# Kernel optimization log

Hardware: AMD Instinct MI355X
Metric: run time of the kernel (lower is better)

Reference implementation:

```python
import jax, jax.numpy as jnp
import numpy as np

N_ENT, N_REL, E_DIM, R_DIM, K, B = 100000, 64, 128, 128, 32, 16384


def _lookup_maxnorm(table, ids):
    # torch nn.Embedding(max_norm=1): rows with L2 norm > 1 are renormed to 1 at lookup
    x = table[ids]
    n = jnp.linalg.norm(x, axis=-1, keepdims=True)
    return x * jnp.minimum(1.0, 1.0 / jnp.maximum(n, 1e-12))


def setup_inputs() -> dict:
    key = jax.random.key(0)
    ks = jax.random.split(key, 10)
    xavier = lambda k, shp: jax.random.uniform(k, shp, jnp.float32, -1.0, 1.0) * np.sqrt(6.0 / (shp[0] + shp[1]))
    return {
        "idx": jax.random.randint(ks[0], (B,), 0, N_ENT),
        "adj_ent": jax.random.randint(ks[1], (N_ENT, K), 0, N_ENT),
        "adj_rel": jax.random.randint(ks[2], (N_ENT, K), 0, N_REL),
        "ent_table": xavier(ks[3], (N_ENT, E_DIM)),
        "rel_table": xavier(ks[4], (N_REL, R_DIM)),
        "Wr_w": xavier(ks[5], (R_DIM, E_DIM)),
        "Wr_b": jnp.zeros((R_DIM,), jnp.float32),
        "W1_w": xavier(ks[6], (E_DIM, E_DIM)),
        "W1_b": jnp.zeros((E_DIM,), jnp.float32),
        "W2_w": xavier(ks[7], (E_DIM, E_DIM)),
        "W2_b": jnp.zeros((E_DIM,), jnp.float32),
    }


def reference(idx, adj_ent, adj_rel, ent_table, rel_table, Wr_w, Wr_b, W1_w, W1_b, W2_w, W2_b):
    idx = jnp.clip(idx, 0, N_ENT - 1)
    e_ids = adj_ent[idx]                      # [B, K]
    r_ids = adj_rel[idx]                      # [B, K]
    t = _lookup_maxnorm(ent_table, e_ids)     # [B, K, E]
    r = _lookup_maxnorm(rel_table, r_ids)     # [B, K, R]
    h = _lookup_maxnorm(ent_table, idx)       # [B, E]
    # GAT message pass
    hr = h @ Wr_w.T + Wr_b                    # [B, R]
    tr = t @ Wr_w.T + Wr_b                    # [B, K, R]
    score = jnp.sum(jnp.tanh(hr[:, None, :] + r) * tr, axis=-1, keepdims=True)  # [B, K, 1]
    att = jax.nn.softmax(score, axis=1)
    Nh = jnp.sum(t * att, axis=1)             # [B, E]
    # Bi-Interaction aggregate
    leaky = lambda x: jax.nn.leaky_relu(x, 0.2)
    return leaky((h + Nh) @ W1_w.T + W1_b) + leaky((h * Nh) @ W2_w.T + W2_b)
```

## Files before the change

### kernel.cpp

```cpp
#include <hip/hip_runtime.h>
#include <hip/hip_fp16.h>
#include <math.h>

#define N_ENT 100000
#define N_REL 64
#define DIM   128
#define KNB   32
#define BATCH 16384
#define STRIPS (N_ENT / 16)

typedef _Float16 f16;
typedef __attribute__((ext_vector_type(2))) _Float16 f16x2;
typedef __attribute__((ext_vector_type(8))) _Float16 f16x8;
typedef __attribute__((ext_vector_type(4))) float floatx4;

__device__ __forceinline__ int clamp_id(int id) {
    return id < 0 ? 0 : (id > N_ENT - 1 ? N_ENT - 1 : id);
}

__device__ __forceinline__ float poly_tanh(float x) {
    const float x2 = x * x;
    return x * fmaf(x2, fmaf(x2, 0.13333334f, -0.33333334f), 1.0f);
}

__device__ __forceinline__ f16x2 h2v(__half2 h) {
    union { __half2 h; f16x2 v; } u; u.h = h; return u.v;
}

__global__ __launch_bounds__(256) void k_small(
    const float* __restrict__ Wr, const float* __restrict__ W1,
    const float* __restrict__ W2, f16* __restrict__ Wr16,
    f16* __restrict__ W116, f16* __restrict__ W216,
    const float* __restrict__ rel, __half2* __restrict__ REL2)
{
    if (blockIdx.x < 64) {
        const int t = blockIdx.x * 256 + threadIdx.x;
        Wr16[t] = (f16)Wr[t];
        W116[t] = (f16)W1[t];
        W216[t] = (f16)W2[t];
    } else {
        const int lane = threadIdx.x & 63;
        const int row  = (blockIdx.x - 64) * 4 + (threadIdx.x >> 6);
        const float2 x = *(const float2*)(rel + row * DIM + 2 * lane);
        float ss = x.x * x.x + x.y * x.y;
        #pragma unroll
        for (int m = 1; m < 64; m <<= 1) ss += __shfl_xor(ss, m);
        const float s = fminf(1.0f, 1.0f / fmaxf(sqrtf(ss), 1e-12f));
        REL2[row * 64 + lane] = __floats2half2_rn(x.x * s, x.y * s);
    }
}

__global__ __launch_bounds__(256, 4) void k_pre(
    const float* __restrict__ ent, const f16* __restrict__ B,
    const float* __restrict__ bias, f16* __restrict__ TR16,
    f16* __restrict__ N16)
{
    __shared__ f16 Bs[32 * 512];
    const int wid  = threadIdx.x >> 6;
    const int lane = threadIdx.x & 63;
    const int m = lane & 15, quad = lane >> 4;

    #pragma unroll
    for (int i = 0; i < 8; ++i) {
        const int s  = wid * 8 + i;
        const int ct = s >> 2, kt = s & 3;
        const f16* gsrc = B + (size_t)(ct * 16 + m) * DIM + kt * 32 + quad * 8;
        __builtin_amdgcn_global_load_lds(
            (const __attribute__((address_space(1))) unsigned int*)gsrc,
            (__attribute__((address_space(3))) unsigned int*)(Bs + s * 512),
            16, 0, 0);
    }

    const int wstrip = (blockIdx.x * 4 + wid) * 2;
    const int s0 = wstrip     < STRIPS ? wstrip     : STRIPS - 1;
    const int s1 = wstrip + 1 < STRIPS ? wstrip + 1 : STRIPS - 1;

    const float* __restrict__ src0 = ent + (size_t)(s0 * 16 + m) * DIM + quad * 8;
    const float* __restrict__ src1 = ent + (size_t)(s1 * 16 + m) * DIM + quad * 8;
    float x0[4][8], x1[4][8];
    #pragma unroll
    for (int kt = 0; kt < 4; ++kt) {
        *(float4*)&x0[kt][0] = *(const float4*)(src0 + kt * 32);
        *(float4*)&x0[kt][4] = *(const float4*)(src0 + kt * 32 + 4);
    }
    #pragma unroll
    for (int kt = 0; kt < 4; ++kt) {
        *(float4*)&x1[kt][0] = *(const float4*)(src1 + kt * 32);
        *(float4*)&x1[kt][4] = *(const float4*)(src1 + kt * 32 + 4);
    }
    __builtin_amdgcn_sched_barrier(0);

    float ss0 = 0.0f;
    #pragma unroll
    for (int kt = 0; kt < 4; ++kt)
        #pragma unroll
        for (int j = 0; j < 8; ++j) ss0 = fmaf(x0[kt][j], x0[kt][j], ss0);
    ss0 += __shfl_xor(ss0, 16);
    ss0 += __shfl_xor(ss0, 32);
    const float sc0 = fminf(1.0f, 1.0f / fmaxf(sqrtf(ss0), 1e-12f));
    f16x8 a0[4];
    {
        f16* __restrict__ ndst = N16 + (size_t)(s0 * 16 + m) * DIM + quad * 8;
        #pragma unroll
        for (int kt = 0; kt < 4; ++kt) {
            f16x8 av;
            #pragma unroll
            for (int j = 0; j < 8; ++j) av[j] = (f16)(x0[kt][j] * sc0);
            a0[kt] = av;
            *(f16x8*)(ndst + kt * 32) = av;
        }
    }

    float ss1 = 0.0f;
    #pragma unroll
    for (int kt = 0; kt < 4; ++kt)
        #pragma unroll
        for (int j = 0; j < 8; ++j) ss1 = fmaf(x1[kt][j], x1[kt][j], ss1);
    ss1 += __shfl_xor(ss1, 16);
    ss1 += __shfl_xor(ss1, 32);
    const float sc1 = fminf(1.0f, 1.0f / fmaxf(sqrtf(ss1), 1e-12f));
    f16x8 a1[4];
    {
        f16* __restrict__ ndst = N16 + (size_t)(s1 * 16 + m) * DIM + quad * 8;
        #pragma unroll
        for (int kt = 0; kt < 4; ++kt) {
            f16x8 av;
            #pragma unroll
            for (int j = 0; j < 8; ++j) av[j] = (f16)(x1[kt][j] * sc1);
            a1[kt] = av;
            *(f16x8*)(ndst + kt * 32) = av;
        }
    }

    __syncthreads();

    #pragma unroll
    for (int ct = 0; ct < 8; ++ct) {
        floatx4 acc0 = {0.0f, 0.0f, 0.0f, 0.0f};
        floatx4 acc1 = {0.0f, 0.0f, 0.0f, 0.0f};
        #pragma unroll
        for (int kt = 0; kt < 4; ++kt) {
            const f16x8 b = *(const f16x8*)(Bs + (ct * 4 + kt) * 512 + lane * 8);
            acc0 = __builtin_amdgcn_mfma_f32_16x16x32_f16(a0[kt], b, acc0, 0, 0, 0);
            acc1 = __builtin_amdgcn_mfma_f32_16x16x32_f16(a1[kt], b, acc1, 0, 0, 0);
        }
        const float bb = bias[ct * 16 + m];
        #pragma unroll
        for (int r = 0; r < 4; ++r) {
            TR16[(size_t)(s0 * 16 + quad * 4 + r) * DIM + ct * 16 + m] = (f16)(acc0[r] + bb);
            TR16[(size_t)(s1 * 16 + quad * 4 + r) * DIM + ct * 16 + m] = (f16)(acc1[r] + bb);
        }
    }
}

__global__ __launch_bounds__(256, 4) void k_sa(
    const int* __restrict__ idx, const int* __restrict__ adj_ent,
    const int* __restrict__ adj_rel, const __half2* __restrict__ TR2,
    const __half2* __restrict__ N2, const __half2* __restrict__ REL2,
    __half2* __restrict__ U2, __half2* __restrict__ V2)
{
    const int wid  = threadIdx.x >> 6;
    const int lane = threadIdx.x & 63;
    const int b = blockIdx.x * 4 + wid;

    const int id = clamp_id(idx[b]);
    const __half2 hr2 = TR2[(size_t)id * 64 + lane];
    const float2 h  = __half22float2(N2[(size_t)id * 64 + lane]);
    const int eL = adj_ent[(size_t)id * KNB + (lane & 31)];
    const int rL = adj_rel[(size_t)id * KNB + (lane & 31)];

    unsigned int tnd[KNB];
    #pragma unroll
    for (int k = 0; k < KNB; ++k) {
        const int e = __builtin_amdgcn_readlane(eL, k);
        tnd[k] = *((const unsigned int*)N2 + (size_t)e * 64 + lane);
    }

    const __half2 C1 = __float2half2_rn(-0.33333334f);
    const __half2 C2 = __float2half2_rn(0.13333334f);
    float p[KNB];
    #pragma unroll
    for (int k = 0; k < KNB; ++k) {
        const int e = __builtin_amdgcn_readlane(eL, k);
        const int r = __builtin_amdgcn_readlane(rL, k);
        const __half2 tr2 = TR2[(size_t)e * 64 + lane];
        const __half2 rn2 = REL2[r * 64 + lane];
        const __half2 x  = __hadd2(hr2, rn2);
        const __half2 xx = __hmul2(x, x);
        __half2 q = __hfma2(xx, C2, C1);
        q = __hmul2(q, xx);
        const __half2 mm = __hfma2(x, q, x);
#if __has_builtin(__builtin_amdgcn_fdot2)
        p[k] = __builtin_amdgcn_fdot2(h2v(mm), h2v(tr2), 0.0f, false);
#else
        const float2 mf = __half22float2(mm);
        const float2 tf = __half22float2(tr2);
        p[k] = mf.x * tf.x + mf.y * tf.y;
#endif
    }

    #pragma unroll
    for (int step = 0; step < 5; ++step) {
        const int half = 16 >> step;
        const int mask = 1 << step;
        const bool hi_lane = (lane & mask) != 0;
        #pragma unroll
        for (int i = 0; i < 16; ++i) {
            if (i >= half) break;
            const float lo = p[i], hi = p[i + half];
            const float send = hi_lane ? lo : hi;
            const float recv = __shfl_xor(send, mask);
            p[i] = (hi_lane ? hi : lo) + recv;
        }
    }
    const float sc = p[0] + __shfl_xor(p[0], 32);

    const float ex = __expf(sc);
    float tt = ex;
    #pragma unroll
    for (int m = 1; m < 32; m <<= 1) tt += __shfl_xor(tt, m);
    const float attL = ex * __builtin_amdgcn_rcpf(tt);

    float nh0 = 0.0f, nh1 = 0.0f;
    #pragma unroll
    for (int k = 0; k < KNB; ++k) {
        const float a = __uint_as_float(
            __builtin_amdgcn_readlane(__float_as_uint(attL), k));
        const float2 t = __half22float2(*(const __half2*)&tnd[k]);
        nh0 = fmaf(a, t.x, nh0);
        nh1 = fmaf(a, t.y, nh1);
    }

    U2[(size_t)b * 64 + lane] = __floats2half2_rn(h.x + nh0, h.y + nh1);
    V2[(size_t)b * 64 + lane] = __floats2half2_rn(h.x * nh0, h.y * nh1);
}

__global__ __launch_bounds__(256, 4) void k_gemm_out(
    const f16* __restrict__ U, const f16* __restrict__ V,
    const f16* __restrict__ W1h, const float* __restrict__ b1,
    const f16* __restrict__ W2h, const float* __restrict__ b2,
    float* __restrict__ out)
{
    const int wid  = threadIdx.x >> 6;
    const int lane = threadIdx.x & 63;
    const int g = blockIdx.x * 4 + wid;
    const int strip = g >> 1;
    const int ct0 = (g & 1) * 4;
    const int row0 = strip * 16;
    const int m = lane & 15, quad = lane >> 4;

    f16x8 au[4], av[4];
    #pragma unroll
    for (int kt = 0; kt < 4; ++kt) {
        au[kt] = *(const f16x8*)(U + (size_t)(row0 + m) * DIM + kt * 32 + quad * 8);
        av[kt] = *(const f16x8*)(V + (size_t)(row0 + m) * DIM + kt * 32 + quad * 8);
    }

    #pragma unroll
    for (int c = 0; c < 4; ++c) {
        const int ct = ct0 + c;
        floatx4 accU = {0.0f, 0.0f, 0.0f, 0.0f};
        floatx4 accV = {0.0f, 0.0f, 0.0f, 0.0f};
        #pragma unroll
        for (int kt = 0; kt < 4; ++kt) {
            const f16x8 bu = *(const f16x8*)(W1h + (size_t)(ct * 16 + m) * DIM + kt * 32 + quad * 8);
            const f16x8 bv = *(const f16x8*)(W2h + (size_t)(ct * 16 + m) * DIM + kt * 32 + quad * 8);
            accU = __builtin_amdgcn_mfma_f32_16x16x32_f16(au[kt], bu, accU, 0, 0, 0);
            accV = __builtin_amdgcn_mfma_f32_16x16x32_f16(av[kt], bv, accV, 0, 0, 0);
        }
        const float bb1 = b1[ct * 16 + m];
        const float bb2 = b2[ct * 16 + m];
        #pragma unroll
        for (int r = 0; r < 4; ++r) {
            const float x = accU[r] + bb1;
            const float y = accV[r] + bb2;
            const float lx = x > 0.0f ? x : 0.2f * x;
            const float ly = y > 0.0f ? y : 0.2f * y;
            out[(size_t)(row0 + quad * 4 + r) * DIM + ct * 16 + m] = lx + ly;
        }
    }
}

extern "C" void kernel_launch(void* const* d_in, const int* in_sizes, int n_in,
                              void* d_out, int out_size, void* d_ws, size_t ws_size,
                              hipStream_t stream) {
    (void)in_sizes; (void)n_in; (void)out_size; (void)ws_size;
    const int*   idx     = (const int*)d_in[0];
    const int*   adj_ent = (const int*)d_in[1];
    const int*   adj_rel = (const int*)d_in[2];
    const float* ent     = (const float*)d_in[3];
    const float* rel     = (const float*)d_in[4];
    const float* Wr_w    = (const float*)d_in[5];
    const float* Wr_b    = (const float*)d_in[6];
    const float* W1_w    = (const float*)d_in[7];
    const float* W1_b    = (const float*)d_in[8];
    const float* W2_w    = (const float*)d_in[9];
    const float* W2_b    = (const float*)d_in[10];
    float* out = (float*)d_out;

    char* ws = (char*)d_ws;
    f16* N16   = (f16*)(ws);
    f16* TR16  = (f16*)(ws + 25600000);
    f16* REL16 = (f16*)(ws + 51200000);
    f16* U16   = (f16*)(ws + 51216384);
    f16* V16   = (f16*)(ws + 55410688);
    f16* Wr16  = (f16*)(ws + 59604992);
    f16* W116  = (f16*)(ws + 59637760);
    f16* W216  = (f16*)(ws + 59670528);

    k_small<<<dim3(80), dim3(256), 0, stream>>>(Wr_w, W1_w, W2_w, Wr16, W116, W216,
                                                rel, (__half2*)REL16);
    k_pre<<<dim3((STRIPS + 7) / 8), dim3(256), 0, stream>>>(ent, Wr16, Wr_b,
                                                            TR16, N16);
    k_sa<<<dim3(BATCH / 4), dim3(256), 0, stream>>>(idx, adj_ent, adj_rel,
                                                    (const __half2*)TR16,
                                                    (const __half2*)N16,
                                                    (const __half2*)REL16,
                                                    (__half2*)U16, (__half2*)V16);
    k_gemm_out<<<dim3(512), dim3(256), 0, stream>>>(U16, V16, W116, W1_b,
                                                    W216, W2_b, out);
}
```

Before: 184.5 us.

## Fuse attention aggregation with output GEMM through swizzled shared memory

Merges the per-row attention/aggregation kernel with the bi-interaction output GEMM. Each 256-thread block now processes 16 batch rows: every wave handles 4 rows sequentially, writes U and V into XOR-swizzled LDS tiles, then after a barrier computes 2 column tiles of the MFMA GEMM. This removes the global round trip for U/V and one kernel launch. In exchange the grid shrinks by 4x to 1024 blocks, and the sequential per-wave loop plus the barrier may reduce latency hiding on the gather-heavy phase.

```diff
diff --git a/kernel.cpp b/kernel.cpp
--- a/kernel.cpp
+++ b/kernel.cpp
@@ -16,11 +16,6 @@
 
 __device__ __forceinline__ int clamp_id(int id) {
     return id < 0 ? 0 : (id > N_ENT - 1 ? N_ENT - 1 : id);
-}
-
-__device__ __forceinline__ float poly_tanh(float x) {
-    const float x2 = x * x;
-    return x * fmaf(x2, fmaf(x2, 0.13333334f, -0.33333334f), 1.0f);
 }
 
 __device__ __forceinline__ f16x2 h2v(__half2 h) {
@@ -153,112 +148,113 @@
     }
 }
 
-__global__ __launch_bounds__(256, 4) void k_sa(
+__global__ __launch_bounds__(256, 4) void k_sag(
     const int* __restrict__ idx, const int* __restrict__ adj_ent,
     const int* __restrict__ adj_rel, const __half2* __restrict__ TR2,
     const __half2* __restrict__ N2, const __half2* __restrict__ REL2,
-    __half2* __restrict__ U2, __half2* __restrict__ V2)
-{
-    const int wid  = threadIdx.x >> 6;
-    const int lane = threadIdx.x & 63;
-    const int b = blockIdx.x * 4 + wid;
-
-    const int id = clamp_id(idx[b]);
-    const __half2 hr2 = TR2[(size_t)id * 64 + lane];
-    const float2 h  = __half22float2(N2[(size_t)id * 64 + lane]);
-    const int eL = adj_ent[(size_t)id * KNB + (lane & 31)];
-    const int rL = adj_rel[(size_t)id * KNB + (lane & 31)];
-
-    unsigned int tnd[KNB];
-    #pragma unroll
-    for (int k = 0; k < KNB; ++k) {
-        const int e = __builtin_amdgcn_readlane(eL, k);
-        tnd[k] = *((const unsigned int*)N2 + (size_t)e * 64 + lane);
-    }
-
-    const __half2 C1 = __float2half2_rn(-0.33333334f);
-    const __half2 C2 = __float2half2_rn(0.13333334f);
-    float p[KNB];
-    #pragma unroll
-    for (int k = 0; k < KNB; ++k) {
-        const int e = __builtin_amdgcn_readlane(eL, k);
-        const int r = __builtin_amdgcn_readlane(rL, k);
-        const __half2 tr2 = TR2[(size_t)e * 64 + lane];
-        const __half2 rn2 = REL2[r * 64 + lane];
-        const __half2 x  = __hadd2(hr2, rn2);
-        const __half2 xx = __hmul2(x, x);
-        __half2 q = __hfma2(xx, C2, C1);
-        q = __hmul2(q, xx);
-        const __half2 mm = __hfma2(x, q, x);
-#if __has_builtin(__builtin_amdgcn_fdot2)
-        p[k] = __builtin_amdgcn_fdot2(h2v(mm), h2v(tr2), 0.0f, false);
-#else
-        const float2 mf = __half22float2(mm);
-        const float2 tf = __half22float2(tr2);
-        p[k] = mf.x * tf.x + mf.y * tf.y;
-#endif
-    }
-
-    #pragma unroll
-    for (int step = 0; step < 5; ++step) {
-        const int half = 16 >> step;
-        const int mask = 1 << step;
-        const bool hi_lane = (lane & mask) != 0;
-        #pragma unroll
-        for (int i = 0; i < 16; ++i) {
-            if (i >= half) break;
-            const float lo = p[i], hi = p[i + half];
-            const float send = hi_lane ? lo : hi;
-            const float recv = __shfl_xor(send, mask);
-            p[i] = (hi_lane ? hi : lo) + recv;
-        }
-    }
-    const float sc = p[0] + __shfl_xor(p[0], 32);
-
-    const float ex = __expf(sc);
-    float tt = ex;
-    #pragma unroll
-    for (int m = 1; m < 32; m <<= 1) tt += __shfl_xor(tt, m);
-    const float attL = ex * __builtin_amdgcn_rcpf(tt);
-
-    float nh0 = 0.0f, nh1 = 0.0f;
-    #pragma unroll
-    for (int k = 0; k < KNB; ++k) {
-        const float a = __uint_as_float(
-            __builtin_amdgcn_readlane(__float_as_uint(attL), k));
-        const float2 t = __half22float2(*(const __half2*)&tnd[k]);
-        nh0 = fmaf(a, t.x, nh0);
-        nh1 = fmaf(a, t.y, nh1);
-    }
-
-    U2[(size_t)b * 64 + lane] = __floats2half2_rn(h.x + nh0, h.y + nh1);
-    V2[(size_t)b * 64 + lane] = __floats2half2_rn(h.x * nh0, h.y * nh1);
-}
-
-__global__ __launch_bounds__(256, 4) void k_gemm_out(
-    const f16* __restrict__ U, const f16* __restrict__ V,
     const f16* __restrict__ W1h, const float* __restrict__ b1,
     const f16* __restrict__ W2h, const float* __restrict__ b2,
     float* __restrict__ out)
 {
+    __shared__ f16 Us[16 * DIM];
+    __shared__ f16 Vs[16 * DIM];
     const int wid  = threadIdx.x >> 6;
     const int lane = threadIdx.x & 63;
-    const int g = blockIdx.x * 4 + wid;
-    const int strip = g >> 1;
-    const int ct0 = (g & 1) * 4;
-    const int row0 = strip * 16;
+    const int row0 = blockIdx.x * 16;
+
+    const __half2 C1 = __float2half2_rn(-0.33333334f);
+    const __half2 C2 = __float2half2_rn(0.13333334f);
+
+    #pragma unroll 1
+    for (int e4 = 0; e4 < 4; ++e4) {
+        const int r = wid * 4 + e4;
+        const int b = row0 + r;
+        const int id = clamp_id(idx[b]);
+        const __half2 hr2 = TR2[(size_t)id * 64 + lane];
+        const float2 h  = __half22float2(N2[(size_t)id * 64 + lane]);
+        const int eL = adj_ent[(size_t)id * KNB + (lane & 31)];
+        const int rL = adj_rel[(size_t)id * KNB + (lane & 31)];
+
+        unsigned int tnd[KNB];
+        #pragma unroll
+        for (int k = 0; k < KNB; ++k) {
+            const int e = __builtin_amdgcn_readlane(eL, k);
+            tnd[k] = *((const unsigned int*)N2 + (size_t)e * 64 + lane);
+        }
+
+        float p[KNB];
+        #pragma unroll
+        for (int k = 0; k < KNB; ++k) {
+            const int e = __builtin_amdgcn_readlane(eL, k);
+            const int rr = __builtin_amdgcn_readlane(rL, k);
+            const __half2 tr2 = TR2[(size_t)e * 64 + lane];
+            const __half2 rn2 = REL2[rr * 64 + lane];
+            const __half2 x  = __hadd2(hr2, rn2);
+            const __half2 xx = __hmul2(x, x);
+            __half2 q = __hfma2(xx, C2, C1);
+            q = __hmul2(q, xx);
+            const __half2 mm = __hfma2(x, q, x);
+#if __has_builtin(__builtin_amdgcn_fdot2)
+            p[k] = __builtin_amdgcn_fdot2(h2v(mm), h2v(tr2), 0.0f, false);
+#else
+            const float2 mf = __half22float2(mm);
+            const float2 tf = __half22float2(tr2);
+            p[k] = mf.x * tf.x + mf.y * tf.y;
+#endif
+        }
+
+        #pragma unroll
+        for (int step = 0; step < 5; ++step) {
+            const int half = 16 >> step;
+            const int mask = 1 << step;
+            const bool hi_lane = (lane & mask) != 0;
+            #pragma unroll
+            for (int i = 0; i < 16; ++i) {
+                if (i >= half) break;
+                const float lo = p[i], hi = p[i + half];
+                const float send = hi_lane ? lo : hi;
+                const float recv = __shfl_xor(send, mask);
+                p[i] = (hi_lane ? hi : lo) + recv;
+            }
+        }
+        const float sc = p[0] + __shfl_xor(p[0], 32);
+
+        const float ex = __expf(sc);
+        float tt = ex;
+        #pragma unroll
+        for (int m2 = 1; m2 < 32; m2 <<= 1) tt += __shfl_xor(tt, m2);
+        const float attL = ex * __builtin_amdgcn_rcpf(tt);
+
+        float nh0 = 0.0f, nh1 = 0.0f;
+        #pragma unroll
+        for (int k = 0; k < KNB; ++k) {
+            const float a = __uint_as_float(
+                __builtin_amdgcn_readlane(__float_as_uint(attL), k));
+            const float2 t = __half22float2(*(const __half2*)&tnd[k]);
+            nh0 = fmaf(a, t.x, nh0);
+            nh1 = fmaf(a, t.y, nh1);
+        }
+
+        const int chunk = lane >> 2;
+        const int boff = r * 256 + ((chunk ^ (r & 7)) << 4) + (lane & 3) * 4;
+        *(__half2*)((char*)Us + boff) = __floats2half2_rn(h.x + nh0, h.y + nh1);
+        *(__half2*)((char*)Vs + boff) = __floats2half2_rn(h.x * nh0, h.y * nh1);
+    }
+
+    __syncthreads();
+
     const int m = lane & 15, quad = lane >> 4;
-
     f16x8 au[4], av[4];
     #pragma unroll
     for (int kt = 0; kt < 4; ++kt) {
-        au[kt] = *(const f16x8*)(U + (size_t)(row0 + m) * DIM + kt * 32 + quad * 8);
-        av[kt] = *(const f16x8*)(V + (size_t)(row0 + m) * DIM + kt * 32 + quad * 8);
-    }
-
-    #pragma unroll
-    for (int c = 0; c < 4; ++c) {
-        const int ct = ct0 + c;
+        const int off = m * 256 + (((kt * 4 + quad) ^ (m & 7)) << 4);
+        au[kt] = *(const f16x8*)((const char*)Us + off);
+        av[kt] = *(const f16x8*)((const char*)Vs + off);
+    }
+
+    #pragma unroll
+    for (int c = 0; c < 2; ++c) {
+        const int ct = wid * 2 + c;
         floatx4 accU = {0.0f, 0.0f, 0.0f, 0.0f};
         floatx4 accV = {0.0f, 0.0f, 0.0f, 0.0f};
         #pragma unroll
@@ -302,8 +298,6 @@
     f16* N16   = (f16*)(ws);
     f16* TR16  = (f16*)(ws + 25600000);
     f16* REL16 = (f16*)(ws + 51200000);
-    f16* U16   = (f16*)(ws + 51216384);
-    f16* V16   = (f16*)(ws + 55410688);
     f16* Wr16  = (f16*)(ws + 59604992);
     f16* W116  = (f16*)(ws + 59637760);
     f16* W216  = (f16*)(ws + 59670528);
@@ -312,11 +306,10 @@
                                                 rel, (__half2*)REL16);
     k_pre<<<dim3((STRIPS + 7) / 8), dim3(256), 0, stream>>>(ent, Wr16, Wr_b,
                                                             TR16, N16);
-    k_sa<<<dim3(BATCH / 4), dim3(256), 0, stream>>>(idx, adj_ent, adj_rel,
-                                                    (const __half2*)TR16,
-                                                    (const __half2*)N16,
-                                                    (const __half2*)REL16,
-                                                    (__half2*)U16, (__half2*)V16);
-    k_gemm_out<<<dim3(512), dim3(256), 0, stream>>>(U16, V16, W116, W1_b,
-                                                    W216, W2_b, out);
-}
+    k_sag<<<dim3(BATCH / 16), dim3(256), 0, stream>>>(idx, adj_ent, adj_rel,
+                                                      (const __half2*)TR16,
+                                                      (const __half2*)N16,
+                                                      (const __half2*)REL16,
+                                                      W116, W1_b, W216, W2_b,
+                                                      out);
+}
```

Result: no change. 181.3 us (-1.8%).
